# Kernel optimization log

Hardware: AMD Instinct MI355X
Metric: run time of the kernel (lower is better)

The kernel has to match this reference:

```python
import jax, jax.numpy as jnp
import numpy as np

B, M, N, Z = 4, 64, 64, 64
IN_DIM, OUT_DIM = 32, 32
MODES1 = MODES2 = MODES3 = 16
HIDDEN = OUT_DIM * 4  # factor=4, n_ff_layers=2
LN_EPS = 1e-5


def setup_inputs() -> dict:
    key = jax.random.key(0)
    ks = jax.random.split(key, 10)
    # xavier-normal-ish scale for (in, out, modes, 2) fourier weights
    fscale = np.sqrt(2.0 / (IN_DIM + OUT_DIM))
    x = jax.random.normal(ks[0], (B, M, N, Z, IN_DIM), dtype=jnp.float32)
    wx = jax.random.normal(ks[1], (IN_DIM, OUT_DIM, MODES1, 2), dtype=jnp.float32) * fscale
    wy = jax.random.normal(ks[2], (IN_DIM, OUT_DIM, MODES2, 2), dtype=jnp.float32) * fscale
    wz = jax.random.normal(ks[3], (IN_DIM, OUT_DIM, MODES3, 2), dtype=jnp.float32) * fscale
    # FeedForward: Linear(OUT_DIM, HIDDEN) + ReLU, then Linear(HIDDEN, OUT_DIM) + LayerNorm
    w0 = jax.random.normal(ks[4], (OUT_DIM, HIDDEN), dtype=jnp.float32) * np.sqrt(1.0 / OUT_DIM)
    b0 = jnp.zeros((HIDDEN,), dtype=jnp.float32)
    w1 = jax.random.normal(ks[5], (HIDDEN, OUT_DIM), dtype=jnp.float32) * np.sqrt(1.0 / HIDDEN)
    b1 = jnp.zeros((OUT_DIM,), dtype=jnp.float32)
    ln_g = jnp.ones((OUT_DIM,), dtype=jnp.float32)
    ln_b = jnp.zeros((OUT_DIM,), dtype=jnp.float32)
    return {"x": x, "wx": wx, "wy": wy, "wz": wz,
            "w0": w0, "b0": b0, "w1": w1, "b1": b1,
            "ln_g": ln_g, "ln_b": ln_b}


def _as_complex(w):
    return w[..., 0] + 1j * w[..., 1]


def _forward_fourier(x, wx, wy, wz):
    # x: [b, m, n, z, i] -> [b, i, m, n, z]
    xt = jnp.transpose(x, (0, 4, 1, 2, 3))
    # --- axis M (dim 2) ---
    ftx = jnp.fft.rfft(xt, axis=2, norm='ortho')  # [b, i, M//2+1, n, z] complex
    ox = jnp.einsum('bixyz,iox->boxyz', ftx[:, :, :MODES1], _as_complex(wx))
    ox = jnp.pad(ox, ((0, 0), (0, 0), (0, M // 2 + 1 - MODES1), (0, 0), (0, 0)))
    xx = jnp.fft.irfft(ox, n=M, axis=2, norm='ortho')
    # --- axis N (dim 3) ---
    fty = jnp.fft.rfft(xt, axis=3, norm='ortho')
    oy = jnp.einsum('bixyz,ioy->boxyz', fty[:, :, :, :MODES2], _as_complex(wy))
    oy = jnp.pad(oy, ((0, 0), (0, 0), (0, 0), (0, N // 2 + 1 - MODES2), (0, 0)))
    xy = jnp.fft.irfft(oy, n=N, axis=3, norm='ortho')
    # --- axis Z (dim 4) ---
    ftz = jnp.fft.rfft(xt, axis=4, norm='ortho')
    oz = jnp.einsum('bixyz,ioz->boxyz', ftz[:, :, :, :, :MODES3], _as_complex(wz))
    oz = jnp.pad(oz, ((0, 0), (0, 0), (0, 0), (0, 0), (0, Z // 2 + 1 - MODES3)))
    xz = jnp.fft.irfft(oz, n=Z, axis=4, norm='ortho')
    out = xx + xy + xz  # [b, o, m, n, z]
    return jnp.transpose(out, (0, 2, 3, 4, 1))  # [b, m, n, z, o]


def reference(x, wx, wy, wz, w0, b0, w1, b1, ln_g, ln_b):
    s = _forward_fourier(x, wx, wy, wz)
    h = jax.nn.relu(s @ w0 + b0)
    y = h @ w1 + b1
    mu = jnp.mean(y, axis=-1, keepdims=True)
    var = jnp.mean((y - mu) ** 2, axis=-1, keepdims=True)
    y = (y - mu) * jax.lax.rsqrt(var + LN_EPS) * ln_g + ln_b
    return y
```

## Files before the change

### kernel.cpp

```cpp
#include <hip/hip_runtime.h>
#include <math.h>

typedef __attribute__((ext_vector_type(8))) short short8v;
typedef __attribute__((ext_vector_type(4))) float float4v;

constexpr float THETA = 6.28318530717958647692f / 64.0f;

constexpr int S_B = 64 * 64 * 64 * 32;
constexpr int S_M = 64 * 64 * 32;
constexpr int S_N = 64 * 32;
constexpr int S_Z = 32;

__device__ __forceinline__ unsigned short f2bf(float f) {
    __bf16 h = (__bf16)f;
    return __builtin_bit_cast(unsigned short, h);
}
__device__ __forceinline__ unsigned int pkbf(float lo, float hi) {
    return (unsigned int)f2bf(lo) | ((unsigned int)f2bf(hi) << 16);
}
__device__ __forceinline__ float bf2f(unsigned int h) {
    return __builtin_bit_cast(float, h << 16);
}

constexpr int WS_TF = 98304, WS_TI = 100352, WS_TOTAL = 102400;

__global__ __launch_bounds__(256)
void setup_frags(const float* __restrict__ wx, const float* __restrict__ wy,
                 const float* __restrict__ wz, unsigned short* __restrict__ W)
{
    int f0 = (blockIdx.x * 256 + threadIdx.x) * 4;
#pragma unroll
    for (int u = 0; u < 4; ++u) {
        int f = f0 + u;
        if (f >= WS_TOTAL) continue;
        unsigned short v;
        if (f < WS_TF) {
            int ax = f >> 15, rem = f & 32767;
            int k = rem >> 11;
            int rem2 = rem & 2047;
            int wt = rem2 >> 10, rt = (rem2 >> 9) & 1, l = (rem2 >> 3) & 63, e = rem2 & 7;
            int o = 16 * rt + (l & 15), i = 8 * (l >> 4) + e;
            const float* w = (ax == 0) ? wx : ((ax == 1) ? wy : wz);
            v = f2bf(w[((i * 32 + o) * 16 + k) * 2 + wt]);
        } else if (f < WS_TI) {
            int rem = f - WS_TF;
            int jt = rem >> 10, s = (rem >> 9) & 1, l = (rem >> 3) & 63, e = rem & 7;
            int kk = l & 15, m = 32 * s + 8 * (l >> 4) + e;
            int jm = (kk * m) & 63;
            float ang = THETA * (float)jm;
            v = f2bf(jt == 0 ? cosf(ang) : sinf(ang));
        } else {
            int rem = f - WS_TI;
            int mt = rem >> 9, l = (rem >> 3) & 63, e = rem & 7;
            int mp = 16 * mt + (l & 15), r = 8 * (l >> 4) + e;
            int k = r & 15;
            float sk = (k == 0) ? (1.0f / 64.0f) : (2.0f / 64.0f);
            int jm = (k * mp) & 63;
            float ang = THETA * (float)jm;
            v = f2bf(r < 16 ? sk * cosf(ang) : -sk * sinf(ang));
        }
        W[f] = v;
    }
}

constexpr int AB_SHORTS = 4096;
__device__ __forceinline__ int ab4(int t, int k, int line, int i) {
    return ((((t * 16 + k) * 4 + line) * 64) + i * 2) ^ (((line ^ k) & 7) << 4);
}
constexpr int P_LS = 1288;
constexpr int P_SHORTS = 4 * P_LS;
__device__ __forceinline__ int p4(int line, int o, int r) {
    return line * P_LS + o * 40 + r;
}

template <int STRIDE>
__device__ __forceinline__ void stageF1(const float* __restrict__ x, long bs,
                                        const unsigned short* __restrict__ tf,
                                        unsigned short* __restrict__ AB,
                                        int lane, int line)
{
    const int gq = lane >> 4, c = lane & 15;
    short8v tfB[2][2];
#pragma unroll
    for (int jt = 0; jt < 2; ++jt)
#pragma unroll
        for (int s = 0; s < 2; ++s)
            tfB[jt][s] = *reinterpret_cast<const short8v*>(tf + ((jt * 2 + s) * 64 + lane) * 8);

    float4v acc[2][2];
#pragma unroll
    for (int rt = 0; rt < 2; ++rt)
#pragma unroll
        for (int jt = 0; jt < 2; ++jt)
            acc[rt][jt] = float4v{0.f, 0.f, 0.f, 0.f};

#pragma unroll
    for (int rt = 0; rt < 2; ++rt) {
        const float* xp = x + bs + 16 * rt + c;
#pragma unroll
        for (int s = 0; s < 2; ++s) {
            short8v a;
#pragma unroll
            for (int e = 0; e < 8; ++e)
                a[e] = (short)f2bf(xp[(long)(32 * s + 8 * gq + e) * STRIDE]);
            acc[rt][0] = __builtin_amdgcn_mfma_f32_16x16x32_bf16(a, tfB[0][s], acc[rt][0], 0, 0, 0);
            acc[rt][1] = __builtin_amdgcn_mfma_f32_16x16x32_bf16(a, tfB[1][s], acc[rt][1], 0, 0, 0);
        }
    }
#pragma unroll
    for (int rt = 0; rt < 2; ++rt)
#pragma unroll
        for (int jt = 0; jt < 2; ++jt) {
            *reinterpret_cast<uint2*>(reinterpret_cast<char*>(AB) + ab4(jt, c, line, 16 * rt + 4 * gq)) =
                make_uint2(pkbf(acc[rt][jt][0], acc[rt][jt][1]), pkbf(acc[rt][jt][2], acc[rt][jt][3]));
        }
}

__device__ __forceinline__ void stageMx4(const unsigned short* __restrict__ wf,
                                         const unsigned short* __restrict__ AB,
                                         unsigned short* __restrict__ P,
                                         int lane, int wave)
{
    const int gq = lane >> 4, c = lane & 15;
    const int t2 = wave >> 1, rt = wave & 1, lc = c & 3;
    for (int k = 0; k < 16; k += 2) {
        float4v acc2[2];
#pragma unroll
        for (int kk = 0; kk < 2; ++kk) {
            const int kc = k + kk;
            short8v aT = *reinterpret_cast<const short8v*>(reinterpret_cast<const char*>(AB) + ab4(0, kc, lc, 8 * gq));
            short8v bT = *reinterpret_cast<const short8v*>(reinterpret_cast<const char*>(AB) + ab4(1, kc, lc, 8 * gq));
            const int w1t = t2 ? 1 : 0, w2t = t2 ? 0 : 1;
            short8v w1 = *reinterpret_cast<const short8v*>(wf + (((kc * 2 + w1t) * 2 + rt) * 64 + lane) * 8);
            short8v w2 = *reinterpret_cast<const short8v*>(wf + (((kc * 2 + w2t) * 2 + rt) * 64 + lane) * 8);
            if (t2) {
                union { short8v s; unsigned int u[4]; } nb;
                nb.s = bT;
#pragma unroll
                for (int j = 0; j < 4; ++j) nb.u[j] ^= 0x80008000u;
                bT = nb.s;
            }
            float4v a2 = float4v{0.f, 0.f, 0.f, 0.f};
            a2 = __builtin_amdgcn_mfma_f32_16x16x32_bf16(w1, aT, a2, 0, 0, 0);
            a2 = __builtin_amdgcn_mfma_f32_16x16x32_bf16(w2, bT, a2, 0, 0, 0);
            acc2[kk] = a2;
        }
        if (c < 4) {
#pragma unroll
            for (int r = 0; r < 4; ++r) {
                *reinterpret_cast<unsigned int*>(&P[p4(c, 16 * rt + 4 * gq + r, 16 * t2 + k)]) =
                    pkbf(acc2[0][r], acc2[1][r]);
            }
        }
    }
}

template <int AXIS>
__device__ __forceinline__ void spectral_body(const float* __restrict__ x,
                                              const unsigned short* __restrict__ wf,
                                              const unsigned short* __restrict__ tf,
                                              const unsigned short* __restrict__ ti,
                                              unsigned short* __restrict__ pw,
                                              unsigned short* __restrict__ AB,
                                              unsigned short* __restrict__ P,
                                              int l, int lane, int wave)
{
    constexpr int stride = (AXIS == 0) ? S_M : S_N;
    const int b = l >> 12, p1 = (l >> 6) & 63, p2 = l & 63;
    const long bs = (AXIS == 0)
        ? (long)b * S_B + (long)p1 * S_N + (long)p2 * S_Z
        : (long)b * S_B + (long)p1 * S_M + (long)p2 * S_Z;
    const int gq = lane >> 4, c = lane & 15;

    stageF1<stride>(x, bs, tf, AB, lane, wave);
    __syncthreads();
    stageMx4(wf, AB, P, lane, wave);
    __syncthreads();

    short8v tiB[4];
#pragma unroll
    for (int mt = 0; mt < 4; ++mt)
        tiB[mt] = *reinterpret_cast<const short8v*>(ti + (mt * 64 + lane) * 8);

    short8v pA[2];
    pA[0] = *reinterpret_cast<const short8v*>(&P[p4(wave, c, 8 * gq)]);
    pA[1] = *reinterpret_cast<const short8v*>(&P[p4(wave, 16 + c, 8 * gq)]);

#pragma unroll
    for (int rt = 0; rt < 2; ++rt)
#pragma unroll
        for (int mt = 0; mt < 4; ++mt) {
            float4v acc = float4v{0.f, 0.f, 0.f, 0.f};
            acc = __builtin_amdgcn_mfma_f32_16x16x32_bf16(pA[rt], tiB[mt], acc, 0, 0, 0);
            const long off = bs + (long)(16 * mt + c) * stride + 16 * rt + 4 * gq;
            *reinterpret_cast<uint2*>(pw + off) =
                make_uint2(pkbf(acc[0], acc[1]), pkbf(acc[2], acc[3]));
        }
}

__global__ __launch_bounds__(256)
void spectral_xy(const float* __restrict__ x,
                 const unsigned short* __restrict__ wf0,
                 const unsigned short* __restrict__ wf1,
                 const unsigned short* __restrict__ tf,
                 const unsigned short* __restrict__ ti,
                 unsigned short* __restrict__ pw1,
                 unsigned short* __restrict__ pw2)
{
    __shared__ __align__(16) unsigned short AB[AB_SHORTS];
    __shared__ __align__(16) unsigned short P[P_SHORTS];
    const int t = threadIdx.x, lane = t & 63, wave = t >> 6;
    if (blockIdx.x < 4096) {
        spectral_body<0>(x, wf0, tf, ti, pw1, AB, P, blockIdx.x * 4 + wave, lane, wave);
    } else {
        spectral_body<1>(x, wf1, tf, ti, pw2, AB, P, (blockIdx.x - 4096) * 4 + wave, lane, wave);
    }
}

template <int AXIS, int MODE>
__global__ __launch_bounds__(256)
void spectral_mfma(const float* __restrict__ x,
                   const unsigned short* __restrict__ wf,
                   const unsigned short* __restrict__ tf,
                   const unsigned short* __restrict__ ti,
                   float* __restrict__ out,
                   unsigned short* __restrict__ pw)
{
    __shared__ __align__(16) unsigned short AB[AB_SHORTS];
    __shared__ __align__(16) unsigned short P[P_SHORTS];

    const int t = threadIdx.x, lane = t & 63, wave = t >> 6;
    const int gq = lane >> 4, c = lane & 15;
    constexpr int stride = (AXIS == 0) ? S_M : S_N;

    const int l = blockIdx.x * 4 + wave;
    const int b = l >> 12, p1 = (l >> 6) & 63, p2 = l & 63;
    const long bs = (AXIS == 0)
        ? (long)b * S_B + (long)p1 * S_N + (long)p2 * S_Z
        : (long)b * S_B + (long)p1 * S_M + (long)p2 * S_Z;

    stageF1<stride>(x, bs, tf, AB, lane, wave);
    __syncthreads();
    stageMx4(wf, AB, P, lane, wave);
    __syncthreads();

    short8v tiB[4];
#pragma unroll
    for (int mt = 0; mt < 4; ++mt)
        tiB[mt] = *reinterpret_cast<const short8v*>(ti + (mt * 64 + lane) * 8);

    short8v pA[2];
    pA[0] = *reinterpret_cast<const short8v*>(&P[p4(wave, c, 8 * gq)]);
    pA[1] = *reinterpret_cast<const short8v*>(&P[p4(wave, 16 + c, 8 * gq)]);

#pragma unroll
    for (int rt = 0; rt < 2; ++rt)
#pragma unroll
        for (int mt = 0; mt < 4; ++mt) {
            float4v acc = float4v{0.f, 0.f, 0.f, 0.f};
            acc = __builtin_amdgcn_mfma_f32_16x16x32_bf16(pA[rt], tiB[mt], acc, 0, 0, 0);
            const long off = bs + (long)(16 * mt + c) * stride + 16 * rt + 4 * gq;
            if (MODE == 0) {
                *reinterpret_cast<float4*>(out + off) = make_float4(acc[0], acc[1], acc[2], acc[3]);
            } else if (MODE == 1) {
                float4 old = *reinterpret_cast<const float4*>(out + off);
                old.x += acc[0]; old.y += acc[1]; old.z += acc[2]; old.w += acc[3];
                *reinterpret_cast<float4*>(out + off) = old;
            } else if (MODE == 2) {
                *reinterpret_cast<uint2*>(pw + off) =
                    make_uint2(pkbf(acc[0], acc[1]), pkbf(acc[2], acc[3]));
            } else {
                uint2 old = *reinterpret_cast<const uint2*>(pw + off);
                const float v0 = bf2f(old.x & 0xffffu) + acc[0];
                const float v1 = bf2f(old.x >> 16)     + acc[1];
                const float v2 = bf2f(old.y & 0xffffu) + acc[2];
                const float v3 = bf2f(old.y >> 16)     + acc[3];
                *reinterpret_cast<uint2*>(pw + off) =
                    make_uint2(pkbf(v0, v1), pkbf(v2, v3));
            }
        }
}

template <int NPART>
__global__ __launch_bounds__(256)
void spectral_fused(const float* __restrict__ x,
                    const unsigned short* __restrict__ wf,
                    const unsigned short* __restrict__ tf,
                    const unsigned short* __restrict__ ti,
                    const float* __restrict__ w0, const float* __restrict__ b0,
                    const float* __restrict__ w1, const float* __restrict__ b1,
                    const float* __restrict__ g,  const float* __restrict__ bb,
                    const unsigned short* __restrict__ pw1,
                    const unsigned short* __restrict__ pw2,
                    const float* __restrict__ pf32,
                    float* __restrict__ out)
{
    __shared__ __align__(16) unsigned short sm[23584];
    constexpr int OP = 8192, OS = 13344;

    const int t = threadIdx.x, lane = t & 63, wave = t >> 6;
    const int gq = lane >> 4, c = lane & 15;

    const int l = blockIdx.x * 4 + wave;
    const int b = l >> 12, p1 = (l >> 6) & 63, p2 = l & 63;
    const long bs = (long)b * S_B + (long)p1 * S_M + (long)p2 * S_N;

    float4 b0q[8];
#pragma unroll
    for (int n = 0; n < 8; ++n)
        b0q[n] = *reinterpret_cast<const float4*>(b0 + 16 * n + 4 * gq);
    float b1v[2], gv[2], bvv[2];
#pragma unroll
    for (int n = 0; n < 2; ++n) { b1v[n] = b1[n * 16 + c]; gv[n] = g[n * 16 + c]; bvv[n] = bb[n * 16 + c]; }

    stageF1<S_Z>(x, bs, tf, sm, lane, wave);
    __syncthreads();
    stageMx4(wf, sm, sm + OP, lane, wave);
    __syncthreads();

    for (int s = t; s < 512; s += 256) {
        const int n = s >> 6, ln = s & 63, g2 = ln >> 4, c2 = ln & 15;
        const int kb = n >> 1, nn = n & 1;
        short8v v0, v1;
#pragma unroll
        for (int e = 0; e < 8; ++e) {
            v0[e] = (short)f2bf(w0[(8 * g2 + e) * 128 + n * 16 + c2]);
            v1[e] = (short)f2bf(w1[(32 * kb + 8 * g2 + e) * 32 + nn * 16 + c2]);
        }
        *reinterpret_cast<short8v*>(&sm[s * 8])        = v0;
        *reinterpret_cast<short8v*>(&sm[4096 + s * 8]) = v1;
    }

    short8v tiB[4];
#pragma unroll
    for (int mt = 0; mt < 4; ++mt)
        tiB[mt] = *reinterpret_cast<const short8v*>(ti + (mt * 64 + lane) * 8);

    {
        short8v pA[2];
        pA[0] = *reinterpret_cast<const short8v*>(&sm[OP + p4(wave, c, 8 * gq)]);
        pA[1] = *reinterpret_cast<const short8v*>(&sm[OP + p4(wave, 16 + c, 8 * gq)]);
#pragma unroll
        for (int rt = 0; rt < 2; ++rt)
#pragma unroll
            for (int mt = 0; mt < 4; ++mt) {
                float4v acc = float4v{0.f, 0.f, 0.f, 0.f};
                acc = __builtin_amdgcn_mfma_f32_16x16x32_bf16(pA[rt], tiB[mt], acc, 0, 0, 0);
                const long off = bs + (long)(16 * mt + c) * S_Z + 16 * rt + 4 * gq;
                float v0, v1, v2, v3;
                if (NPART == 0) {
                    float4 old = *reinterpret_cast<const float4*>(pf32 + off);
                    v0 = old.x + acc[0]; v1 = old.y + acc[1];
                    v2 = old.z + acc[2]; v3 = old.w + acc[3];
                } else {
                    uint2 pv = *reinterpret_cast<const uint2*>(pw1 + off);
                    v0 = bf2f(pv.x & 0xffffu) + acc[0];
                    v1 = bf2f(pv.x >> 16)     + acc[1];
                    v2 = bf2f(pv.y & 0xffffu) + acc[2];
                    v3 = bf2f(pv.y >> 16)     + acc[3];
                    if (NPART == 2) {
                        uint2 qv = *reinterpret_cast<const uint2*>(pw2 + off);
                        v0 += bf2f(qv.x & 0xffffu);
                        v1 += bf2f(qv.x >> 16);
                        v2 += bf2f(qv.y & 0xffffu);
                        v3 += bf2f(qv.y >> 16);
                    }
                }
                const int si = OS + (wave * 64 + 16 * mt + c) * 40 + 16 * rt + 4 * gq;
                *reinterpret_cast<uint2*>(&sm[si]) = make_uint2(pkbf(v0, v1), pkbf(v2, v3));
            }
    }
    __syncthreads();

    const int Hb = OS + wave * 2560;

    short8v af[4];
#pragma unroll
    for (int f = 0; f < 4; ++f)
        af[f] = *reinterpret_cast<const short8v*>(&sm[OS + (wave * 64 + 16 * f + c) * 40 + 8 * gq]);

    float4v Y[4][2];
#pragma unroll
    for (int f = 0; f < 4; ++f)
#pragma unroll
        for (int n = 0; n < 2; ++n)
            Y[f][n] = float4v{b1v[n], b1v[n], b1v[n], b1v[n]};

#pragma unroll
    for (int kb = 0; kb < 4; ++kb) {
#pragma unroll
        for (int nn = 0; nn < 2; ++nn) {
            const int n = 2 * kb + nn;
            const short8v wv = *reinterpret_cast<const short8v*>(&sm[(n * 64 + lane) * 8]);
#pragma unroll
            for (int f = 0; f < 4; ++f) {
                float4v hacc = float4v{b0q[n].x, b0q[n].y, b0q[n].z, b0q[n].w};
                hacc = __builtin_amdgcn_mfma_f32_16x16x32_bf16(wv, af[f], hacc, 0, 0, 0);
                const float h0 = fmaxf(hacc[0], 0.f), h1 = fmaxf(hacc[1], 0.f);
                const float h2 = fmaxf(hacc[2], 0.f), h3 = fmaxf(hacc[3], 0.f);
                *reinterpret_cast<uint2*>(&sm[Hb + (16 * f + c) * 40 + 16 * nn + 4 * gq]) =
                    make_uint2(pkbf(h0, h1), pkbf(h2, h3));
            }
        }
        const short8v wva = *reinterpret_cast<const short8v*>(&sm[4096 + ((kb * 2 + 0) * 64 + lane) * 8]);
        const short8v wvb = *reinterpret_cast<const short8v*>(&sm[4096 + ((kb * 2 + 1) * 64 + lane) * 8]);
#pragma unroll
        for (int f = 0; f < 4; ++f) {
            const short8v a2 = *reinterpret_cast<const short8v*>(&sm[Hb + (16 * f + c) * 40 + 8 * gq]);
            Y[f][0] = __builtin_amdgcn_mfma_f32_16x16x32_bf16(a2, wva, Y[f][0], 0, 0, 0);
            Y[f][1] = __builtin_amdgcn_mfma_f32_16x16x32_bf16(a2, wvb, Y[f][1], 0, 0, 0);
        }
    }

#pragma unroll
    for (int f = 0; f < 4; ++f) {
        float smv[4], sq[4];
#pragma unroll
        for (int r = 0; r < 4; ++r) {
            const float v0 = Y[f][0][r], v1 = Y[f][1][r];
            smv[r] = v0 + v1;
            sq[r]  = v0 * v0 + v1 * v1;
        }
#pragma unroll
        for (int mask = 1; mask <= 8; mask <<= 1) {
#pragma unroll
            for (int r = 0; r < 4; ++r) {
                smv[r] += __shfl_xor(smv[r], mask);
                sq[r]  += __shfl_xor(sq[r], mask);
            }
        }
#pragma unroll
        for (int r = 0; r < 4; ++r) {
            const float mu = smv[r] * (1.0f / 32.0f);
            const float var = sq[r] * (1.0f / 32.0f) - mu * mu;
            const float rs = rsqrtf(var + 1e-5f);
            float* op = out + bs + (long)(16 * f + 4 * gq + r) * 32;
            op[c]      = (Y[f][0][r] - mu) * rs * gv[0] + bvv[0];
            op[16 + c] = (Y[f][1][r] - mu) * rs * gv[1] + bvv[1];
        }
    }
}

extern "C" void kernel_launch(void* const* d_in, const int* in_sizes, int n_in,
                              void* d_out, int out_size, void* d_ws, size_t ws_size,
                              hipStream_t stream)
{
    const float* x    = (const float*)d_in[0];
    const float* wx   = (const float*)d_in[1];
    const float* wy   = (const float*)d_in[2];
    const float* wz   = (const float*)d_in[3];
    const float* w0   = (const float*)d_in[4];
    const float* b0   = (const float*)d_in[5];
    const float* w1   = (const float*)d_in[6];
    const float* b1   = (const float*)d_in[7];
    const float* ln_g = (const float*)d_in[8];
    const float* ln_b = (const float*)d_in[9];
    float* out = (float*)d_out;

    unsigned short* wsf = (unsigned short*)d_ws;

    const size_t PART_OFF   = 262144;
    const size_t PART_BYTES = (size_t)33554432 * 2;
    unsigned short* pw1 = (unsigned short*)((char*)d_ws + PART_OFF);
    unsigned short* pw2 = (unsigned short*)((char*)d_ws + PART_OFF + PART_BYTES);
    const int tier = (ws_size >= PART_OFF + 2 * PART_BYTES) ? 2
                   : (ws_size >= PART_OFF + PART_BYTES)     ? 1 : 0;

    setup_frags<<<100, 256, 0, stream>>>(wx, wy, wz, wsf);

    if (tier == 2) {
        spectral_xy<<<8192, 256, 0, stream>>>(x, wsf + 0 * 32768, wsf + 1 * 32768,
                                              wsf + WS_TF, wsf + WS_TI, pw1, pw2);
        spectral_fused<2><<<4096, 256, 0, stream>>>(x, wsf + 2 * 32768, wsf + WS_TF, wsf + WS_TI,
                                                    w0, b0, w1, b1, ln_g, ln_b, pw1, pw2, out, out);
    } else if (tier == 1) {
        spectral_mfma<0, 2><<<4096, 256, 0, stream>>>(x, wsf + 0 * 32768, wsf + WS_TF, wsf + WS_TI, out, pw1);
        spectral_mfma<1, 3><<<4096, 256, 0, stream>>>(x, wsf + 1 * 32768, wsf + WS_TF, wsf + WS_TI, out, pw1);
        spectral_fused<1><<<4096, 256, 0, stream>>>(x, wsf + 2 * 32768, wsf + WS_TF, wsf + WS_TI,
                                                    w0, b0, w1, b1, ln_g, ln_b, pw1, pw1, out, out);
    } else {
        spectral_mfma<0, 0><<<4096, 256, 0, stream>>>(x, wsf + 0 * 32768, wsf + WS_TF, wsf + WS_TI, out, pw1);
        spectral_mfma<1, 1><<<4096, 256, 0, stream>>>(x, wsf + 1 * 32768, wsf + WS_TF, wsf + WS_TI, out, pw1);
        spectral_fused<0><<<4096, 256, 0, stream>>>(x, wsf + 2 * 32768, wsf + WS_TF, wsf + WS_TI,
                                                    w0, b0, w1, b1, ln_g, ln_b, pw1, pw1, out, out);
    }
}
```

Baseline: 225.9 us.

## Batch strided x loads before MFMA and split merged spectral_xy kernel

stageF1 now issues all 32 strided global loads of x into registers before any bf16 conversion or MFMA, so more loads are in flight at once. The merged spectral_xy launch (one 8192-block grid that branches between the M and N axes) is replaced by two separate spectral_mfma launches writing pw1 and pw2. spectral_mfma also gets a minimum-occupancy launch bound of 4, which caps register use. The extra live registers from the batched loads may collide with that cap and cause spills, and the split adds one kernel launch.

```diff
diff --git a/kernel.cpp b/kernel.cpp
--- a/kernel.cpp
+++ b/kernel.cpp
@@ -87,6 +87,17 @@
         for (int s = 0; s < 2; ++s)
             tfB[jt][s] = *reinterpret_cast<const short8v*>(tf + ((jt * 2 + s) * 64 + lane) * 8);
 
+    float xr[2][2][8];
+#pragma unroll
+    for (int rt = 0; rt < 2; ++rt) {
+        const float* xp = x + bs + 16 * rt + c;
+#pragma unroll
+        for (int s = 0; s < 2; ++s)
+#pragma unroll
+            for (int e = 0; e < 8; ++e)
+                xr[rt][s][e] = xp[(long)(32 * s + 8 * gq + e) * STRIDE];
+    }
+
     float4v acc[2][2];
 #pragma unroll
     for (int rt = 0; rt < 2; ++rt)
@@ -95,18 +106,17 @@
             acc[rt][jt] = float4v{0.f, 0.f, 0.f, 0.f};
 
 #pragma unroll
-    for (int rt = 0; rt < 2; ++rt) {
-        const float* xp = x + bs + 16 * rt + c;
+    for (int rt = 0; rt < 2; ++rt)
 #pragma unroll
         for (int s = 0; s < 2; ++s) {
             short8v a;
 #pragma unroll
             for (int e = 0; e < 8; ++e)
-                a[e] = (short)f2bf(xp[(long)(32 * s + 8 * gq + e) * STRIDE]);
+                a[e] = (short)f2bf(xr[rt][s][e]);
             acc[rt][0] = __builtin_amdgcn_mfma_f32_16x16x32_bf16(a, tfB[0][s], acc[rt][0], 0, 0, 0);
             acc[rt][1] = __builtin_amdgcn_mfma_f32_16x16x32_bf16(a, tfB[1][s], acc[rt][1], 0, 0, 0);
         }
-    }
+
 #pragma unroll
     for (int rt = 0; rt < 2; ++rt)
 #pragma unroll
@@ -155,70 +165,8 @@
     }
 }
 
-template <int AXIS>
-__device__ __forceinline__ void spectral_body(const float* __restrict__ x,
-                                              const unsigned short* __restrict__ wf,
-                                              const unsigned short* __restrict__ tf,
-                                              const unsigned short* __restrict__ ti,
-                                              unsigned short* __restrict__ pw,
-                                              unsigned short* __restrict__ AB,
-                                              unsigned short* __restrict__ P,
-                                              int l, int lane, int wave)
-{
-    constexpr int stride = (AXIS == 0) ? S_M : S_N;
-    const int b = l >> 12, p1 = (l >> 6) & 63, p2 = l & 63;
-    const long bs = (AXIS == 0)
-        ? (long)b * S_B + (long)p1 * S_N + (long)p2 * S_Z
-        : (long)b * S_B + (long)p1 * S_M + (long)p2 * S_Z;
-    const int gq = lane >> 4, c = lane & 15;
-
-    stageF1<stride>(x, bs, tf, AB, lane, wave);
-    __syncthreads();
-    stageMx4(wf, AB, P, lane, wave);
-    __syncthreads();
-
-    short8v tiB[4];
-#pragma unroll
-    for (int mt = 0; mt < 4; ++mt)
-        tiB[mt] = *reinterpret_cast<const short8v*>(ti + (mt * 64 + lane) * 8);
-
-    short8v pA[2];
-    pA[0] = *reinterpret_cast<const short8v*>(&P[p4(wave, c, 8 * gq)]);
-    pA[1] = *reinterpret_cast<const short8v*>(&P[p4(wave, 16 + c, 8 * gq)]);
-
-#pragma unroll
-    for (int rt = 0; rt < 2; ++rt)
-#pragma unroll
-        for (int mt = 0; mt < 4; ++mt) {
-            float4v acc = float4v{0.f, 0.f, 0.f, 0.f};
-            acc = __builtin_amdgcn_mfma_f32_16x16x32_bf16(pA[rt], tiB[mt], acc, 0, 0, 0);
-            const long off = bs + (long)(16 * mt + c) * stride + 16 * rt + 4 * gq;
-            *reinterpret_cast<uint2*>(pw + off) =
-                make_uint2(pkbf(acc[0], acc[1]), pkbf(acc[2], acc[3]));
-        }
-}
-
-__global__ __launch_bounds__(256)
-void spectral_xy(const float* __restrict__ x,
-                 const unsigned short* __restrict__ wf0,
-                 const unsigned short* __restrict__ wf1,
-                 const unsigned short* __restrict__ tf,
-                 const unsigned short* __restrict__ ti,
-                 unsigned short* __restrict__ pw1,
-                 unsigned short* __restrict__ pw2)
-{
-    __shared__ __align__(16) unsigned short AB[AB_SHORTS];
-    __shared__ __align__(16) unsigned short P[P_SHORTS];
-    const int t = threadIdx.x, lane = t & 63, wave = t >> 6;
-    if (blockIdx.x < 4096) {
-        spectral_body<0>(x, wf0, tf, ti, pw1, AB, P, blockIdx.x * 4 + wave, lane, wave);
-    } else {
-        spectral_body<1>(x, wf1, tf, ti, pw2, AB, P, (blockIdx.x - 4096) * 4 + wave, lane, wave);
-    }
-}
-
 template <int AXIS, int MODE>
-__global__ __launch_bounds__(256)
+__global__ __launch_bounds__(256, 4)
 void spectral_mfma(const float* __restrict__ x,
                    const unsigned short* __restrict__ wf,
                    const unsigned short* __restrict__ tf,
@@ -469,8 +417,8 @@
     setup_frags<<<100, 256, 0, stream>>>(wx, wy, wz, wsf);
 
     if (tier == 2) {
-        spectral_xy<<<8192, 256, 0, stream>>>(x, wsf + 0 * 32768, wsf + 1 * 32768,
-                                              wsf + WS_TF, wsf + WS_TI, pw1, pw2);
+        spectral_mfma<0, 2><<<4096, 256, 0, stream>>>(x, wsf + 0 * 32768, wsf + WS_TF, wsf + WS_TI, out, pw1);
+        spectral_mfma<1, 2><<<4096, 256, 0, stream>>>(x, wsf + 1 * 32768, wsf + WS_TF, wsf + WS_TI, out, pw2);
         spectral_fused<2><<<4096, 256, 0, stream>>>(x, wsf + 2 * 32768, wsf + WS_TF, wsf + WS_TI,
                                                     w0, b0, w1, b1, ln_g, ln_b, pw1, pw2, out, out);
     } else if (tier == 1) {
```

Measured after the change: 234.4 us. +3.7%, slower.
